# Optimization experiments

Measured on AMD Instinct MI355X. Metric: run time of the kernel, lower is better.

The kernel has to match this reference:

```python
import jax, jax.numpy as jnp
import numpy as np

NUM_NODES = 100000
NUM_EDGES = 1600000
EMBED_DIM = 128
NUM_CLASSES = 2
NUM_LAYERS = 3


def setup_inputs() -> dict:
    key = jax.random.key(0)
    k_row, k_col, k_val, k_emb, k_a, k_w, k_b = jax.random.split(key, 7)
    node_indices = jnp.arange(NUM_NODES, dtype=jnp.int64 if jax.config.read('jax_enable_x64') else jnp.int32)
    adj_row = jax.random.randint(k_row, (NUM_EDGES,), 0, NUM_NODES)
    adj_col = jax.random.randint(k_col, (NUM_EDGES,), 0, NUM_NODES)
    # symmetric-normalized-ish positive edge weights
    adj_val = jax.random.uniform(k_val, (NUM_EDGES,), dtype=jnp.float32) * (1.0 / 16.0)
    embedding = jax.random.normal(k_emb, (NUM_NODES, EMBED_DIM), dtype=jnp.float32)
    alpha = jnp.ones((NUM_LAYERS + 1,), dtype=jnp.float32) / (NUM_LAYERS + 1)
    W = jax.random.normal(k_w, (EMBED_DIM, NUM_CLASSES), dtype=jnp.float32) * 0.05
    b = jnp.zeros((NUM_CLASSES,), dtype=jnp.float32)
    return {
        'node_indices': node_indices, 'adj_row': adj_row, 'adj_col': adj_col,
        'adj_val': adj_val, 'embedding': embedding, 'alpha': alpha, 'W': W, 'b': b,
    }


def reference(node_indices, adj_row, adj_col, adj_val, embedding, alpha, W, b):
    # x: [N, D] embedding lookup
    x = embedding[node_indices]
    a = jax.nn.softmax(alpha)
    # alpha-weighted running sum over propagation layers (dropout in eval mode = identity)
    acc = a[0] * x
    cur = x
    for i in range(NUM_LAYERS):
        # sparse SpMM: out[r] += val * cur[c] for each edge (r, c)
        msgs = adj_val[:, None] * cur[adj_col]          # [E, D]
        cur = jax.ops.segment_sum(msgs, adj_row, num_segments=NUM_NODES)
        acc = acc + a[i + 1] * cur
    return acc @ W + b  # [N, num_classes]
```

## Files before the change

kernel.cpp:

```cpp
#include <hip/hip_runtime.h>

#define GD(x,y) (((x)+(y)-1)/(y))

#define SH    10
#define BPR   (1 << SH)
#define G1    256
#define BS    256
#define KSPL  24
#define CAPSH 15
#define CAP   (1 << CAPSH)

static __device__ __forceinline__ float2 ntload2(const float2* p){
    unsigned long long u = __builtin_nontemporal_load((const unsigned long long*)p);
    return *(float2*)&u;
}
static __device__ __forceinline__ void ntstore2(float2* p, float2 v){
    __builtin_nontemporal_store(*(unsigned long long*)&v, (unsigned long long*)p);
}

__global__ void init_k(int* __restrict__ cursor, int NBK,
                       const float* __restrict__ alpha, float* __restrict__ a, int na){
    int t = threadIdx.x;
    if (t < NBK) cursor[t] = t << CAPSH;
    if (t == 0){
        float m = alpha[0];
        for (int i = 1; i < na; ++i) m = fmaxf(m, alpha[i]);
        float s = 0.f;
        for (int i = 0; i < na; ++i){ float e = expf(alpha[i] - m); a[i] = e; s += e; }
        float inv = 1.f / s;
        for (int i = 0; i < na; ++i) a[i] *= inv;
    }
}

__global__ void fillf_k(const int* __restrict__ row, const int* __restrict__ col,
                        const float* __restrict__ val, int* __restrict__ cursor,
                        int2* __restrict__ sep, int E, int NBK, int chunk){
    __shared__ int h[128];
    __shared__ int curb[128];
    int t = threadIdx.x;
    for (int i = t; i < NBK; i += BS) h[i] = 0;
    __syncthreads();
    int s = blockIdx.x * chunk, e = min(E, s + chunk);
    for (int i = s + t; i < e; i += BS)
        atomicAdd(&h[row[i] >> SH], 1);
    __syncthreads();
    if (t < NBK) curb[t] = (h[t] > 0) ? atomicAdd(&cursor[t], h[t]) : 0;
    __syncthreads();
    for (int i = s + t; i < e; i += BS){
        int r = row[i];
        int b = r >> SH;
        int pos = atomicAdd(&curb[b], 1);
        int2 pk;
        pk.x = col[i] | ((r & (BPR - 1)) << 17);
        pk.y = __float_as_int(val[i]);
        sep[pos] = pk;
    }
}

__global__ void proj_k(const float* __restrict__ emb, const int* __restrict__ idx,
                       const float* __restrict__ W, const float* __restrict__ b,
                       const float* __restrict__ a, float* __restrict__ y,
                       float* __restrict__ out, int N){
    int t = blockIdx.x * blockDim.x + threadIdx.x;
    int w = t >> 6;
    int lane = t & 63;
    int n = w * 2 + (lane >> 5);
    if (n >= N) return;
    int sl = lane & 31;
    float4 x = ((const float4*)(emb + (size_t)idx[n] * 128))[sl];
    int d0 = 4 * sl;
    float s0 = x.x * W[d0*2]   + x.y * W[d0*2+2] + x.z * W[d0*2+4] + x.w * W[d0*2+6];
    float s1 = x.x * W[d0*2+1] + x.y * W[d0*2+3] + x.z * W[d0*2+5] + x.w * W[d0*2+7];
    #pragma unroll
    for (int off = 16; off; off >>= 1){
        s0 += __shfl_down(s0, off, 32);
        s1 += __shfl_down(s1, off, 32);
    }
    if (sl == 0){
        float c = a[0];
        ((float2*)y)[n]   = make_float2(s0, s1);
        ((float2*)out)[n] = make_float2(b[0] + c * s0, b[1] + c * s1);
    }
}

__global__ void spmm_k(const int* __restrict__ cursor, const int2* __restrict__ sep,
                       const float* __restrict__ yin, float* __restrict__ partial,
                       int NBK){
    __shared__ float accx[BPR];
    __shared__ float accy[BPR];
    int b  = blockIdx.x / KSPL;
    int sp = blockIdx.x % KSPL;
    int t  = threadIdx.x;
    for (int j = t; j < BPR; j += BS){ accx[j] = 0.f; accy[j] = 0.f; }
    __syncthreads();
    int s = b << CAPSH;
    int e = cursor[b];
    int len = e - s, per = GD(len, KSPL);
    int cs = s + sp * per, ce = min(e, cs + per);
    int i = cs + t;
    for (; i + 3 * BS < ce; i += 4 * BS){
        int2 p0 = sep[i], p1 = sep[i + BS], p2 = sep[i + 2*BS], p3 = sep[i + 3*BS];
        float2 m0 = ((const float2*)yin)[p0.x & 0x1FFFF];
        float2 m1 = ((const float2*)yin)[p1.x & 0x1FFFF];
        float2 m2 = ((const float2*)yin)[p2.x & 0x1FFFF];
        float2 m3 = ((const float2*)yin)[p3.x & 0x1FFFF];
        float v0 = __int_as_float(p0.y), v1 = __int_as_float(p1.y);
        float v2 = __int_as_float(p2.y), v3 = __int_as_float(p3.y);
        atomicAdd(&accx[p0.x >> 17], v0 * m0.x); atomicAdd(&accy[p0.x >> 17], v0 * m0.y);
        atomicAdd(&accx[p1.x >> 17], v1 * m1.x); atomicAdd(&accy[p1.x >> 17], v1 * m1.y);
        atomicAdd(&accx[p2.x >> 17], v2 * m2.x); atomicAdd(&accy[p2.x >> 17], v2 * m2.y);
        atomicAdd(&accx[p3.x >> 17], v3 * m3.x); atomicAdd(&accy[p3.x >> 17], v3 * m3.y);
    }
    for (; i < ce; i += BS){
        int2 pk = sep[i];
        float v = __int_as_float(pk.y);
        float2 m = ((const float2*)yin)[pk.x & 0x1FFFF];
        atomicAdd(&accx[pk.x >> 17], v * m.x);
        atomicAdd(&accy[pk.x >> 17], v * m.y);
    }
    __syncthreads();
    float2* dst = (float2*)partial + (size_t)(b * KSPL + sp) * BPR;
    for (int j = t; j < BPR; j += BS)
        ntstore2(&dst[j], make_float2(accx[j], accy[j]));
}

__global__ void comb_k(const float* __restrict__ partial, const float* __restrict__ a,
                       int ai, float* __restrict__ ynext, float* __restrict__ out,
                       int N, int store){
    int n = blockIdx.x * blockDim.x + threadIdx.x;
    if (n >= N) return;
    int b = n >> SH, j = n & (BPR - 1);
    const float2* p = (const float2*)partial + (size_t)b * KSPL * BPR + j;
    float sx = 0.f, sy = 0.f;
    #pragma unroll
    for (int sp = 0; sp < KSPL; ++sp){
        float2 v = ntload2(&p[(size_t)sp * BPR]);
        sx += v.x; sy += v.y;
    }
    if (store) ((float2*)ynext)[n] = make_float2(sx, sy);
    float c = a[ai];
    float2 o = ((float2*)out)[n];
    o.x += c * sx; o.y += c * sy;
    ((float2*)out)[n] = o;
}

extern "C" void kernel_launch(void* const* d_in, const int* in_sizes, int n_in,
                              void* d_out, int out_size, void* d_ws, size_t ws_size,
                              hipStream_t stream) {
    const int*   node_idx = (const int*)  d_in[0];
    const int*   adj_row  = (const int*)  d_in[1];
    const int*   adj_col  = (const int*)  d_in[2];
    const float* adj_val  = (const float*)d_in[3];
    const float* emb      = (const float*)d_in[4];
    const float* alpha    = (const float*)d_in[5];
    const float* W        = (const float*)d_in[6];
    const float* b        = (const float*)d_in[7];
    float* out = (float*)d_out;

    const int N = in_sizes[0];
    const int E = in_sizes[1];
    const int L = in_sizes[5] - 1;
    const int NBK = GD(N, BPR);
    const int chunk = GD(E, G1);

    char* w = (char*)d_ws;
    float* yA     = (float*)w;  w += (size_t)N * 2 * 4;
    float* yB     = (float*)w;  w += (size_t)N * 2 * 4;
    float* partial= (float*)w;  w += (size_t)NBK * KSPL * BPR * 2 * 4;
    int2*  sep    = (int2*)w;   w += (size_t)NBK * CAP * 8;
    int*   cursor = (int*)w;    w += 1024;
    float* a      = (float*)w;

    init_k<<<1, 128, 0, stream>>>(cursor, NBK, alpha, a, L + 1);
    fillf_k<<<G1, BS, 0, stream>>>(adj_row, adj_col, adj_val, cursor, sep, E, NBK, chunk);

    proj_k<<<GD(N * 32, 256), 256, 0, stream>>>(emb, node_idx, W, b, a, yA, out, N);

    float* ysrc = yA;
    float* ydst = yB;
    for (int i = 0; i < L; ++i){
        spmm_k<<<NBK * KSPL, BS, 0, stream>>>(cursor, sep, ysrc, partial, NBK);
        comb_k<<<GD(N, 256), 256, 0, stream>>>(partial, a, i + 1, ydst, out,
                                               N, (i < L - 1) ? 1 : 0);
        float* tmp = ysrc; ysrc = ydst; ydst = tmp;
    }
}
```

Measured before the change: 128.6 us.

## Stage bucketed edges in shared memory and grid over fixed-size chunks

The bucketing kernel now runs many blocks, each covering a fixed 2048-edge chunk instead of 256 large chunks. Edges are loaded with vector int4/float4 reads and sorted by bucket into shared memory, then written out contiguously per bucket, so the global scatter is mostly coalesced. This aims to cut the cost of scattered 8-byte global writes and to raise parallelism in the fill stage. In exchange it adds a serial prefix scan by one thread, more shared memory per block, and more global atomics on the cursor array.

```diff
diff --git a/kernel.cpp b/kernel.cpp
--- a/kernel.cpp
+++ b/kernel.cpp
@@ -4,11 +4,11 @@
 
 #define SH    10
 #define BPR   (1 << SH)
-#define G1    256
 #define BS    256
 #define KSPL  24
 #define CAPSH 15
 #define CAP   (1 << CAPSH)
+#define CHUNK 2048
 
 static __device__ __forceinline__ float2 ntload2(const float2* p){
     unsigned long long u = __builtin_nontemporal_load((const unsigned long long*)p);
@@ -34,26 +34,66 @@
 
 __global__ void fillf_k(const int* __restrict__ row, const int* __restrict__ col,
                         const float* __restrict__ val, int* __restrict__ cursor,
-                        int2* __restrict__ sep, int E, int NBK, int chunk){
-    __shared__ int h[128];
-    __shared__ int curb[128];
+                        int2* __restrict__ sep, int E, int NBK){
+    __shared__ int2 staged[CHUNK];
+    __shared__ unsigned char bid[CHUNK];
+    __shared__ int h[128], lstart[128], gbase[128], lcur[128];
     int t = threadIdx.x;
+    int s = blockIdx.x * CHUNK;
+    int e = min(E, s + CHUNK);
+    int cnt = e - s;
     for (int i = t; i < NBK; i += BS) h[i] = 0;
     __syncthreads();
-    int s = blockIdx.x * chunk, e = min(E, s + chunk);
-    for (int i = s + t; i < e; i += BS)
-        atomicAdd(&h[row[i] >> SH], 1);
-    __syncthreads();
-    if (t < NBK) curb[t] = (h[t] > 0) ? atomicAdd(&cursor[t], h[t]) : 0;
-    __syncthreads();
-    for (int i = s + t; i < e; i += BS){
-        int r = row[i];
-        int b = r >> SH;
-        int pos = atomicAdd(&curb[b], 1);
-        int2 pk;
-        pk.x = col[i] | ((r & (BPR - 1)) << 17);
-        pk.y = __float_as_int(val[i]);
-        sep[pos] = pk;
+    for (int base = s + t * 4; base < e; base += BS * 4){
+        if (base + 3 < e){
+            int4 r4 = *(const int4*)(row + base);
+            atomicAdd(&h[r4.x >> SH], 1);
+            atomicAdd(&h[r4.y >> SH], 1);
+            atomicAdd(&h[r4.z >> SH], 1);
+            atomicAdd(&h[r4.w >> SH], 1);
+        } else {
+            for (int j = 0; j < 4 && base + j < e; ++j)
+                atomicAdd(&h[row[base + j] >> SH], 1);
+        }
+    }
+    __syncthreads();
+    if (t == 0){
+        int run = 0;
+        for (int i = 0; i < NBK; ++i){ lstart[i] = run; run += h[i]; }
+    }
+    __syncthreads();
+    if (t < NBK){
+        lcur[t] = lstart[t];
+        gbase[t] = (h[t] > 0) ? atomicAdd(&cursor[t], h[t]) : 0;
+    }
+    __syncthreads();
+    for (int base = s + t * 4; base < e; base += BS * 4){
+        int  r[4]; int c[4]; float v[4];
+        int  m = min(4, e - base);
+        if (m == 4){
+            int4 r4 = *(const int4*)(row + base);
+            int4 c4 = *(const int4*)(col + base);
+            float4 v4 = *(const float4*)(val + base);
+            r[0]=r4.x; r[1]=r4.y; r[2]=r4.z; r[3]=r4.w;
+            c[0]=c4.x; c[1]=c4.y; c[2]=c4.z; c[3]=c4.w;
+            v[0]=v4.x; v[1]=v4.y; v[2]=v4.z; v[3]=v4.w;
+        } else {
+            for (int j = 0; j < m; ++j){ r[j]=row[base+j]; c[j]=col[base+j]; v[j]=val[base+j]; }
+        }
+        for (int j = 0; j < m; ++j){
+            int b = r[j] >> SH;
+            int lp = atomicAdd(&lcur[b], 1);
+            int2 pk;
+            pk.x = c[j] | ((r[j] & (BPR - 1)) << 17);
+            pk.y = __float_as_int(v[j]);
+            staged[lp] = pk;
+            bid[lp] = (unsigned char)b;
+        }
+    }
+    __syncthreads();
+    for (int idx = t; idx < cnt; idx += BS){
+        int b = bid[idx];
+        sep[gbase[b] + (idx - lstart[b])] = staged[idx];
     }
 }
 
@@ -161,7 +201,7 @@
     const int E = in_sizes[1];
     const int L = in_sizes[5] - 1;
     const int NBK = GD(N, BPR);
-    const int chunk = GD(E, G1);
+    const int GF  = GD(E, CHUNK);
 
     char* w = (char*)d_ws;
     float* yA     = (float*)w;  w += (size_t)N * 2 * 4;
@@ -172,7 +212,7 @@
     float* a      = (float*)w;
 
     init_k<<<1, 128, 0, stream>>>(cursor, NBK, alpha, a, L + 1);
-    fillf_k<<<G1, BS, 0, stream>>>(adj_row, adj_col, adj_val, cursor, sep, E, NBK, chunk);
+    fillf_k<<<GF, BS, 0, stream>>>(adj_row, adj_col, adj_val, cursor, sep, E, NBK);
 
     proj_k<<<GD(N * 32, 256), 256, 0, stream>>>(emb, node_idx, W, b, a, yA, out, N);
 
```

Measured after the change: 125.8 us. 2.1% less time.
